# Kernel optimization log

Measured on AMD Instinct MI355X. Metric: run time of the kernel, lower is better.

Reference implementation:

```python
import jax, jax.numpy as jnp
import numpy as np

B, T, V, D = 256, 128, 32000, 512
DT = 0.04
CUBIC = 0.008
LAMBDA = 0.1
SIGNAL_SCALE = 0.5
NORM_EPS = 1e-8       # state_norm_eps
SIG_EPS = 1e-6        # signal_eps
SLOW_DECAY = 0.05
SLOW_LR = 0.05
W_FAST = 1.0
W_SLOW = 0.3
CONV_STEPS = 4
LN_EPS = 1e-5


def make_diffusion_matrix(dim):
    rng = np.random.default_rng(42)
    q, _ = np.linalg.qr(rng.standard_normal((dim, dim)).astype(np.float64))
    u = rng.random(dim)
    eig = -0.2 - (0.05 + 0.3 * u)
    return jnp.asarray((q * eig) @ q.T, dtype=jnp.float32)


def setup_inputs() -> dict:
    key = jax.random.key(0)
    k1, k2, k3 = jax.random.split(key, 3)
    tokens = jax.random.randint(k1, (B, T), 0, V)
    embed = jax.random.normal(k2, (V, D), dtype=jnp.float32) * 0.02
    readout_w = jax.random.normal(k3, (V, D), dtype=jnp.float32) * 0.02
    diffusion = make_diffusion_matrix(D)
    gamma = jnp.float32(0.2)
    beta = jnp.float32(0.75)
    return {"tokens": tokens, "embed": embed, "readout_w": readout_w,
            "diffusion": diffusion, "gamma": gamma, "beta": beta}


def _layernorm(x):
    mu = jnp.mean(x, axis=-1, keepdims=True)
    var = jnp.mean((x - mu) ** 2, axis=-1, keepdims=True)
    return (x - mu) / jnp.sqrt(var + LN_EPS)


def _norm(x):
    return jnp.linalg.norm(x, axis=-1, keepdims=True)


def _context_vector(fast, slow):
    combined = W_FAST * fast + W_SLOW * slow
    fn = _norm(fast)
    cn = _norm(combined)
    fast_dir = fast / (fn + SIG_EPS)
    comb_dir = combined / (cn + SIG_EPS)
    return jnp.where(fn > 1e-8, fast_dir,
                     jnp.where(cn > 1e-8, comb_dir, jnp.zeros_like(fast)))


def _step_state(state, signal, diffusion, beta):
    c = state - jnp.mean(state, axis=-1, keepdims=True)
    drift = (state @ diffusion.T + CUBIC * jnp.tanh(c)
             + beta * (SIGNAL_SCALE * signal) - LAMBDA * state)
    s = state + DT * drift
    s = jnp.nan_to_num(s, nan=0.0, posinf=0.0, neginf=0.0)
    s = s / (_norm(s) + NORM_EPS)
    return jnp.clip(s, -10.0, 10.0)


def reference(tokens, embed, readout_w, diffusion, gamma, beta):
    # tokens: [B,T] int; states: [B,D]
    fast0 = jnp.zeros((tokens.shape[0], D), dtype=embed.dtype)
    slow0 = jnp.zeros_like(fast0)

    def token_step(carry, tok):
        fast, slow = carry
        emb = _layernorm(embed[tok])                       # [B,D]
        base = emb / jnp.maximum(_norm(emb), 1e-12)
        ctx = _context_vector(fast, slow)
        sig = base + gamma * ctx
        sig = sig / (_norm(sig) + SIG_EPS)
        for _ in range(CONV_STEPS):
            fast = _step_state(fast, sig, diffusion, beta)
        slow = (1.0 - SLOW_DECAY) * slow + SLOW_LR * fast
        sn = _norm(slow)
        slow = jnp.where(sn > 0.5, slow * (0.5 / (sn + 1e-12)), slow)
        return (fast, slow), None

    (fast, slow), _ = jax.lax.scan(token_step, (fast0, slow0), tokens.T)
    combined = W_FAST * fast + W_SLOW * slow               # [B,D]
    logits = combined @ readout_w.T                        # [B,V]
    return logits
```

## Files before the change

kernel.cpp:

```cpp
#include <hip/hip_runtime.h>
#include <math.h>

#define DDIM 512
#define TLEN 128
#define RB   8
#define NWG  32
#define VDIM 32000
#define NWAVE 8
#define SR   528

typedef _Float16 f16x8 __attribute__((ext_vector_type(8)));
typedef float    f32x4 __attribute__((ext_vector_type(4)));
typedef _Float16 h2    __attribute__((ext_vector_type(2)));

__device__ __forceinline__ unsigned int pkh2(float a, float b) {
  h2 v; v.x = (_Float16)a; v.y = (_Float16)b;
  return __builtin_bit_cast(unsigned int, v);
}
__device__ __forceinline__ float h2f(unsigned short h) {
  return (float)__builtin_bit_cast(_Float16, h);
}
__device__ __forceinline__ unsigned short f2h(float f) {
  return __builtin_bit_cast(unsigned short, (_Float16)f);
}
__device__ __forceinline__ float tanh_fast(float x) {
#if __has_builtin(__builtin_amdgcn_exp2f) && __has_builtin(__builtin_amdgcn_rcpf)
  const float e = __builtin_amdgcn_exp2f(x * 2.885390081777927f);
  return 1.f - 2.f * __builtin_amdgcn_rcpf(e + 1.f);
#else
  const float e = exp2f(x * 2.885390081777927f);
  return 1.f - 2.f / (e + 1.f);
#endif
}
__device__ __forceinline__ f32x4 unpk4(uint2 u) {
  f32x4 r;
  r[0] = h2f((unsigned short)(u.x & 0xffff));
  r[1] = h2f((unsigned short)(u.x >> 16));
  r[2] = h2f((unsigned short)(u.y & 0xffff));
  r[3] = h2f((unsigned short)(u.y >> 16));
  return r;
}

__device__ __forceinline__ void wg_barrier() {
  asm volatile("s_waitcnt lgkmcnt(0)" ::: "memory");
  __builtin_amdgcn_s_barrier();
  asm volatile("" ::: "memory");
}

__global__ __launch_bounds__(256) void pack_diffusion(
    const float* __restrict__ A, uint4* __restrict__ pk)
{
  const int slot = blockIdx.x * 256 + threadIdx.x;
  const int l  = slot & 63;
  const int fr = slot >> 6;
  const int kt = fr & 15;
  const int it = fr >> 4;
  const float* src = A + (size_t)(it * 16 + (l & 15)) * DDIM + kt * 32 + (l >> 4) * 8;
  pk[slot] = make_uint4(pkh2(src[0], src[1]), pkh2(src[2], src[3]),
                        pkh2(src[4], src[5]), pkh2(src[6], src[7]));
}

__global__ __launch_bounds__(512) void precompute_mubi(
    const int*   __restrict__ tokens,
    const float* __restrict__ embed,
    float4*      __restrict__ mubi)
{
  const int idx = blockIdx.x * 8 + (threadIdx.x >> 6);
  const int l   = threadIdx.x & 63;
  const int b   = idx >> 7;
  const int t   = idx & 127;
  const int tok = tokens[b * TLEN + t];
  float s1 = 0.f, s2 = 0.f;
  #pragma unroll
  for (int e = 0; e < 8; ++e) {
    const float v = embed[(size_t)tok * DDIM + l + e * 64];
    s1 += v; s2 += v * v;
  }
  #pragma unroll
  for (int off = 32; off >= 1; off >>= 1) {
    s1 += __shfl_xor(s1, off);
    s2 += __shfl_xor(s2, off);
  }
  if (l == 0) {
    const float mu = s1 * (1.f / DDIM);
    float var = s2 * (1.f / DDIM) - mu * mu;
    var = fmaxf(var, 0.f);
    const float inv  = rsqrtf(var + 1e-5f);
    const float n2y  = (float)DDIM * var / (var + 1e-5f);
    const float invn = 1.f / fmaxf(sqrtf(n2y), 1e-12f);
    const float bi   = inv * invn;
    const float b2   = n2y * invn * invn;
    mubi[idx] = make_float4(mu, bi, b2, 0.f);
  }
}

#define PF(B_, KT_)                                                          \
  {                                                                          \
    _Pragma("unroll")                                                        \
    for (int mt = 0; mt < 4; ++mt)                                           \
      B_[mt] = apw[(size_t)(mt * 16 + (KT_)) * 64];                          \
  }
#define USE(B_, KT_)                                                         \
  {                                                                          \
    const f16x8 bf = *(const f16x8*)&srow[rp][rl * SR + (KT_) * 32 + g * 8]; \
    _Pragma("unroll")                                                        \
    for (int mt = 0; mt < 4; ++mt)                                           \
      C[mt] = __builtin_amdgcn_mfma_f32_16x16x32_f16(                        \
          __builtin_bit_cast(f16x8, B_[mt]), bf, C[mt], 0, 0, 0);            \
  }
#define USE_AR(KT_)                                                          \
  {                                                                          \
    const f16x8 bf = *(const f16x8*)&srow[rp][rl * SR + (KT_) * 32 + g * 8]; \
    _Pragma("unroll")                                                        \
    for (int mt = 0; mt < 4; ++mt)                                           \
      C[mt] = __builtin_amdgcn_mfma_f32_16x16x32_f16(                        \
          __builtin_bit_cast(f16x8, AR[KT_][mt]), bf, C[mt], 0, 0, 0);       \
  }
#define USE_LD(KT_)                                                          \
  {                                                                          \
    const f16x8 bf = *(const f16x8*)&srow[rp][rl * SR + (KT_) * 32 + g * 8]; \
    _Pragma("unroll")                                                        \
    for (int mt = 0; mt < 4; ++mt) {                                         \
      const uint4 af = ares[((w * 4 + mt) * 4 + ((KT_) - 4)) * 64 + l];      \
      C[mt] = __builtin_amdgcn_mfma_f32_16x16x32_f16(                        \
          __builtin_bit_cast(f16x8, af), bf, C[mt], 0, 0, 0);                \
    }                                                                        \
  }

__global__ __launch_bounds__(512, 1) void attractor_recurrence(
    const int*    __restrict__ tokens,
    const float*  __restrict__ embed,
    const uint4*  __restrict__ Apk,
    const float4* __restrict__ mubi,
    const float*  __restrict__ gamma_p,
    const float*  __restrict__ beta_p,
    float*        __restrict__ comb_out)
{
  const int tid   = threadIdx.x;
  const int w     = tid >> 6;
  const int l     = tid & 63;
  const int g     = l >> 4;
  const int n     = l & 15;
  const int rl    = n & 7;
  const int hi    = (n >> 3) & 1;
  const int row0  = blockIdx.x * RB;
  const int wbase = w * 64;

  __shared__ unsigned short srow[2][RB * SR];
  __shared__ unsigned short forceh[RB * SR];
  __shared__ float4 redc[2][NWAVE][RB];
  __shared__ float4 redt[NWAVE][2];
  __shared__ float2 carry[RB];
  __shared__ float4 mb[RB];
  __shared__ uint4  ares[32 * 4 * 64];

  for (int x = tid; x < RB * SR; x += 512) { srow[0][x] = 0; srow[1][x] = 0; }
  for (int x = tid; x < 32 * 4 * 64; x += 512) {
    const int it = x >> 8;
    const int kr = (x >> 6) & 3;
    const int ll = x & 63;
    ares[x] = Apk[(size_t)(it * 16 + 4 + kr) * 64 + ll];
  }

  const uint4* apw = Apk + (size_t)(w * 64) * 64 + l;
  uint4 AR[4][4];
  #pragma unroll
  for (int kt = 0; kt < 4; ++kt)
    #pragma unroll
    for (int mt = 0; mt < 4; ++mt)
      AR[kt][mt] = apw[(size_t)(mt * 16 + kt) * 64];

  const float gamma = gamma_p[0];
  const float bss   = beta_p[0] * 0.5f;

  float fs[2][4];
  float sl[2][4];
  #pragma unroll
  for (int mtl = 0; mtl < 2; ++mtl)
    #pragma unroll
    for (int q = 0; q < 4; ++q) { fs[mtl][q] = 0.f; sl[mtl][q] = 0.f; }
  float S_reg = 0.f, S2_reg = 0.f, SX_reg = 0.f;
  float sl2 = 0.f;

  float evc[8];
  #pragma unroll
  for (int r = 0; r < 8; ++r) {
    const int tok = tokens[(row0 + r) * TLEN + 0];
    evc[r] = embed[(size_t)tok * DDIM + tid];
  }

  __syncthreads();

  uint4 A0[4], A1[4], A2[4];
  PF(A0, 8); PF(A1, 9); PF(A2, 10);

  for (int t = 0; t < TLEN; ++t) {
    const int tn = (t + 1 < TLEN) ? t + 1 : t;
    float evn[8];
    #pragma unroll
    for (int r = 0; r < 8; ++r) {
      const int tok = tokens[(row0 + r) * TLEN + tn];
      evn[r] = embed[(size_t)tok * DDIM + tid];
    }
    if (tid < 8) mb[tid] = mubi[(size_t)(row0 + tid) * TLEN + t];
    float pr[8];
    #pragma unroll
    for (int r = 0; r < 8; ++r)
      pr[r] = evc[r] * h2f(srow[0][r * SR + tid]);
    #pragma unroll
    for (int off = 32; off >= 1; off >>= 1)
      #pragma unroll
      for (int q = 0; q < 8; ++q)
        pr[q] += __shfl_xor(pr[q], off);
    if (l == 0) {
      redt[w][0] = make_float4(pr[0], pr[1], pr[2], pr[3]);
      redt[w][1] = make_float4(pr[4], pr[5], pr[6], pr[7]);
    }
    if (tid < 8) carry[tid] = make_float2(S_reg, S2_reg);
    if (t > 0) {
      const float sq3   = sqrtf(S2_reg);
      const float ispn3 = 1.f / (sq3 + 1e-8f);
      const float fn3   = sq3 * ispn3;
      const float sdf   = SX_reg * ispn3;
      const float sn2   = 0.9025f * sl2 + 0.095f * sdf + 0.0025f * fn3 * fn3;
      const float sn    = sqrtf(fmaxf(sn2, 0.f));
      const float scale = (sn > 0.5f) ? 0.5f / (sn + 1e-12f) : 1.f;
      sl2 = sn2 * scale * scale;
      #pragma unroll
      for (int mtl = 0; mtl < 2; ++mtl)
        #pragma unroll
        for (int q = 0; q < 4; ++q)
          sl[mtl][q] = (0.95f * sl[mtl][q] + 0.05f * fs[mtl][q] * ispn3) * scale;
    }
    wg_barrier();

    {
      float rs[8];
      #pragma unroll
      for (int q = 0; q < 8; ++q) rs[q] = 0.f;
      #pragma unroll
      for (int wv = 0; wv < NWAVE; ++wv) {
        const float4 v0 = redt[wv][0];
        const float4 v1 = redt[wv][1];
        rs[0] += v0.x; rs[1] += v0.y; rs[2] += v0.z; rs[3] += v0.w;
        rs[4] += v1.x; rs[5] += v1.y; rs[6] += v1.z; rs[7] += v1.w;
      }
      #pragma unroll
      for (int r = 0; r < 8; ++r) {
        const float2 cy  = carry[r];
        const float4 mbr = mb[r];
        const float sq   = sqrtf(cy.y);
        const float ispr = 1.f / (sq + 1e-8f);
        const float fno  = sq * ispr;
        const float invf = 1.f / (fno + 1e-6f);
        const float qr   = ispr * invf;
        const float mu   = mbr.x;
        const float bi   = mbr.y;
        const float b2   = mbr.z;
        const float sctx = qr * cy.x;
        const float bdot = bi * (qr * rs[r] - mu * sctx);
        const float cn2  = qr * qr * cy.y;
        const float sg2  = b2 + 2.f * gamma * bdot + gamma * gamma * cn2;
        const float isig = 1.f / (sqrtf(fmaxf(sg2, 0.f)) + 1e-6f);
        const float ctx  = qr * h2f(srow[0][r * SR + tid]);
        forceh[r * SR + tid] = f2h(bss * ((evc[r] - mu) * bi + gamma * ctx) * isig);
      }
    }
    wg_barrier();

    #pragma unroll 1
    for (int k = 0; k < 4; ++k) {
      const int  rp   = k & 1;
      const int  wp   = rp ^ 1;
      const bool last = (k == 3);

      f32x4 C[4];
      #pragma unroll
      for (int mt = 0; mt < 4; ++mt) C[mt] = (f32x4){0.f, 0.f, 0.f, 0.f};

      USE_AR(0); USE_AR(1); USE_AR(2); USE_AR(3);
      USE_LD(4); USE_LD(5); USE_LD(6); USE_LD(7);
      USE(A0,  8); PF(A0, 11);
      USE(A1,  9); PF(A1, 12);
      USE(A2, 10); PF(A2, 13);
      USE(A0, 11); PF(A0, 14);
      USE(A1, 12); PF(A1, 15);
      USE(A2, 13); PF(A2, 10);
      USE(A0, 14); PF(A0,  8);
      USE(A1, 15); PF(A1,  9);

      const float ispn  = 1.f / (sqrtf(S2_reg) + 1e-8f);
      const float smean = S_reg * ispn * (1.f / DDIM);
      f32x4 Cs[2];
      Cs[0] = hi ? C[2] : C[0];
      Cs[1] = hi ? C[3] : C[1];
      const int i0base = wbase + hi * 32 + g * 4;
      float vs = 0.f, v2 = 0.f, vx = 0.f;
      #pragma unroll
      for (int mtl = 0; mtl < 2; ++mtl) {
        const int i0 = i0base + mtl * 16;
        const f32x4 ff = unpk4(*(const uint2*)&forceh[rl * SR + i0]);
        #pragma unroll
        for (int q = 0; q < 4; ++q) {
          const float s   = fs[mtl][q] * ispn;
          const float th  = tanh_fast(s - smean);
          const float dr  = Cs[mtl][q] * ispn + 0.008f * th + ff[q] - 0.1f * s;
          const float spv = fmaf(0.04f, dr, s);
          fs[mtl][q] = spv;
          vs += spv; v2 += spv * spv;
          if (last) vx += sl[mtl][q] * spv;
        }
      }
      vs += __shfl_xor(vs, 8);  v2 += __shfl_xor(v2, 8);  vx += __shfl_xor(vx, 8);
      vs += __shfl_xor(vs, 16); v2 += __shfl_xor(v2, 16); vx += __shfl_xor(vx, 16);
      vs += __shfl_xor(vs, 32); v2 += __shfl_xor(v2, 32); vx += __shfl_xor(vx, 32);

      #pragma unroll
      for (int mtl = 0; mtl < 2; ++mtl) {
        const int i0 = i0base + mtl * 16;
        uint2 pkv;
        pkv.x = pkh2(fs[mtl][0], fs[mtl][1]);
        pkv.y = pkh2(fs[mtl][2], fs[mtl][3]);
        *(uint2*)&srow[wp][rl * SR + i0] = pkv;
      }
      if (l < 8) redc[rp][w][l] = make_float4(vs, v2, vx, 0.f);
      wg_barrier();
      float S = 0.f, S2 = 0.f, SX = 0.f;
      #pragma unroll
      for (int wv = 0; wv < NWAVE; ++wv) {
        const float4 v = redc[rp][wv][rl];
        S += v.x; S2 += v.y; SX += v.z;
      }
      S_reg = S; S2_reg = S2; SX_reg = SX;
    }

    #pragma unroll
    for (int r = 0; r < 8; ++r) evc[r] = evn[r];
  }

  {
    const float sq3   = sqrtf(S2_reg);
    const float ispn3 = 1.f / (sq3 + 1e-8f);
    const float fn3   = sq3 * ispn3;
    const float sdf   = SX_reg * ispn3;
    const float sn2   = 0.9025f * sl2 + 0.095f * sdf + 0.0025f * fn3 * fn3;
    const float sn    = sqrtf(fmaxf(sn2, 0.f));
    const float scale = (sn > 0.5f) ? 0.5f / (sn + 1e-12f) : 1.f;
    const int i0base = wbase + hi * 32 + g * 4;
    #pragma unroll
    for (int mtl = 0; mtl < 2; ++mtl) {
      const int i0 = i0base + mtl * 16;
      float4 o;
      #pragma unroll
      for (int q = 0; q < 4; ++q) {
        const float f = fs[mtl][q] * ispn3;
        const float s = (0.95f * sl[mtl][q] + 0.05f * f) * scale;
        ((float*)&o)[q] = f + 0.3f * s;
      }
      *(float4*)&comb_out[(size_t)(row0 + rl) * DDIM + i0] = o;
    }
  }
}

#define KC  32
#define LDT 132

__global__ __launch_bounds__(256) void logits_gemm(
    const float* __restrict__ comb,
    const float* __restrict__ W,
    float*       __restrict__ out)
{
  __shared__ float wt[KC * LDT];
  __shared__ float ct[KC * LDT];

  const int tid = threadIdx.x;
  const int v0  = blockIdx.x * 128;
  const int b0  = blockIdx.y * 128;
  const int tb  = tid >> 4;
  const int tv  = tid & 15;

  float acc[8][8];
  #pragma unroll
  for (int a = 0; a < 8; ++a)
    #pragma unroll
    for (int b = 0; b < 8; ++b) acc[a][b] = 0.f;

  for (int kk = 0; kk < DDIM; kk += KC) {
    #pragma unroll
    for (int it = 0; it < 4; ++it) {
      const int l4  = tid + it * 256;
      const int row = l4 >> 3;
      const int k4  = (l4 & 7) << 2;
      const float4 gw = *(const float4*)&W[(size_t)(v0 + row) * DDIM + kk + k4];
      const float4 gc = *(const float4*)&comb[(size_t)(b0 + row) * DDIM + kk + k4];
      wt[(k4 + 0) * LDT + row] = gw.x;
      wt[(k4 + 1) * LDT + row] = gw.y;
      wt[(k4 + 2) * LDT + row] = gw.z;
      wt[(k4 + 3) * LDT + row] = gw.w;
      ct[(k4 + 0) * LDT + row] = gc.x;
      ct[(k4 + 1) * LDT + row] = gc.y;
      ct[(k4 + 2) * LDT + row] = gc.z;
      ct[(k4 + 3) * LDT + row] = gc.w;
    }
    __syncthreads();

    for (int kx = 0; kx < KC; ++kx) {
      const float4 c0 = *(const float4*)&ct[kx * LDT + tb * 8];
      const float4 c1 = *(const float4*)&ct[kx * LDT + tb * 8 + 4];
      const float4 w0 = *(const float4*)&wt[kx * LDT + tv * 8];
      const float4 w1 = *(const float4*)&wt[kx * LDT + tv * 8 + 4];
      const float cw[8] = {c0.x, c0.y, c0.z, c0.w, c1.x, c1.y, c1.z, c1.w};
      const float wv[8] = {w0.x, w0.y, w0.z, w0.w, w1.x, w1.y, w1.z, w1.w};
      #pragma unroll
      for (int ib = 0; ib < 8; ++ib)
        #pragma unroll
        for (int iv = 0; iv < 8; ++iv)
          acc[ib][iv] = fmaf(cw[ib], wv[iv], acc[ib][iv]);
    }
    __syncthreads();
  }

  #pragma unroll
  for (int ib = 0; ib < 8; ++ib) {
    const size_t base = (size_t)(b0 + tb * 8 + ib) * VDIM + v0 + tv * 8;
    *(float4*)&out[base]     = make_float4(acc[ib][0], acc[ib][1], acc[ib][2], acc[ib][3]);
    *(float4*)&out[base + 4] = make_float4(acc[ib][4], acc[ib][5], acc[ib][6], acc[ib][7]);
  }
}

extern "C" void kernel_launch(void* const* d_in, const int* in_sizes, int n_in,
                              void* d_out, int out_size, void* d_ws, size_t ws_size,
                              hipStream_t stream) {
  const int*   tokens    = (const int*)d_in[0];
  const float* embed     = (const float*)d_in[1];
  const float* readout_w = (const float*)d_in[2];
  const float* diffusion = (const float*)d_in[3];
  const float* gamma_p   = (const float*)d_in[4];
  const float* beta_p    = (const float*)d_in[5];

  float*  comb = (float*)d_ws;
  uint4*  Apk  = (uint4*)((char*)d_ws + 512 * 1024);
  float4* mubi = (float4*)((char*)d_ws + 1024 * 1024);

  hipLaunchKernelGGL(pack_diffusion, dim3(128), dim3(256), 0, stream,
                     diffusion, Apk);
  hipLaunchKernelGGL(precompute_mubi, dim3(256 * TLEN / 8), dim3(512), 0, stream,
                     tokens, embed, mubi);
  hipLaunchKernelGGL(attractor_recurrence, dim3(NWG), dim3(512), 0, stream,
                     tokens, embed, Apk, mubi, gamma_p, beta_p, comb);
  hipLaunchKernelGGL(logits_gemm, dim3(VDIM / 128, 256 / 128), dim3(256), 0, stream,
                     comb, readout_w, (float*)d_out);
}
```

Measured before the change: 3.784 ms.

## Split recurrence state columns across paired workgroups with flag-based global exchange

The recurrence kernel now runs on 64 workgroups via a cooperative launch, each pair of workgroups owning one 8-row batch group and splitting the 512 state columns in half. Each workgroup keeps half of the diffusion matrix (registers plus LDS), computes half of the matvec per step, and then exchanges its fp16 state half and partial norm sums with its partner through global memory, using release/acquire flags and spin-waiting. This halves the per-workgroup MFMA work and diffusion-matrix streaming on the serial critical path. In exchange it adds a global-memory round trip and cross-workgroup synchronisation on each of the 512 inner steps.

```diff
diff --git a/kernel.cpp b/kernel.cpp
--- a/kernel.cpp
+++ b/kernel.cpp
@@ -4,10 +4,10 @@
 #define DDIM 512
 #define TLEN 128
 #define RB   8
-#define NWG  32
 #define VDIM 32000
 #define NWAVE 8
 #define SR   528
+#define PAYB 4608
 
 typedef _Float16 f16x8 __attribute__((ext_vector_type(8)));
 typedef float    f32x4 __attribute__((ext_vector_type(4)));
@@ -88,31 +88,15 @@
     const float inv  = rsqrtf(var + 1e-5f);
     const float n2y  = (float)DDIM * var / (var + 1e-5f);
     const float invn = 1.f / fmaxf(sqrtf(n2y), 1e-12f);
-    const float bi   = inv * invn;
-    const float b2   = n2y * invn * invn;
-    mubi[idx] = make_float4(mu, bi, b2, 0.f);
-  }
-}
-
-#define PF(B_, KT_)                                                          \
-  {                                                                          \
-    _Pragma("unroll")                                                        \
-    for (int mt = 0; mt < 4; ++mt)                                           \
-      B_[mt] = apw[(size_t)(mt * 16 + (KT_)) * 64];                          \
-  }
-#define USE(B_, KT_)                                                         \
-  {                                                                          \
-    const f16x8 bf = *(const f16x8*)&srow[rp][rl * SR + (KT_) * 32 + g * 8]; \
-    _Pragma("unroll")                                                        \
-    for (int mt = 0; mt < 4; ++mt)                                           \
-      C[mt] = __builtin_amdgcn_mfma_f32_16x16x32_f16(                        \
-          __builtin_bit_cast(f16x8, B_[mt]), bf, C[mt], 0, 0, 0);            \
-  }
+    mubi[idx] = make_float4(mu, inv * invn, n2y * invn * invn, 0.f);
+  }
+}
+
 #define USE_AR(KT_)                                                          \
   {                                                                          \
     const f16x8 bf = *(const f16x8*)&srow[rp][rl * SR + (KT_) * 32 + g * 8]; \
     _Pragma("unroll")                                                        \
-    for (int mt = 0; mt < 4; ++mt)                                           \
+    for (int mt = 0; mt < 2; ++mt)                                           \
       C[mt] = __builtin_amdgcn_mfma_f32_16x16x32_f16(                        \
           __builtin_bit_cast(f16x8, AR[KT_][mt]), bf, C[mt], 0, 0, 0);       \
   }
@@ -120,21 +104,23 @@
   {                                                                          \
     const f16x8 bf = *(const f16x8*)&srow[rp][rl * SR + (KT_) * 32 + g * 8]; \
     _Pragma("unroll")                                                        \
-    for (int mt = 0; mt < 4; ++mt) {                                         \
-      const uint4 af = ares[((w * 4 + mt) * 4 + ((KT_) - 4)) * 64 + l];      \
+    for (int mt = 0; mt < 2; ++mt) {                                         \
+      const uint4 af = ares[((w * 2 + mt) * 8 + ((KT_) - 8)) * 64 + l];      \
       C[mt] = __builtin_amdgcn_mfma_f32_16x16x32_f16(                        \
           __builtin_bit_cast(f16x8, af), bf, C[mt], 0, 0, 0);                \
     }                                                                        \
   }
 
-__global__ __launch_bounds__(512, 1) void attractor_recurrence(
+__global__ __launch_bounds__(512, 1) void attractor_coop(
     const int*    __restrict__ tokens,
     const float*  __restrict__ embed,
     const uint4*  __restrict__ Apk,
     const float4* __restrict__ mubi,
     const float*  __restrict__ gamma_p,
     const float*  __restrict__ beta_p,
-    float*        __restrict__ comb_out)
+    float*        __restrict__ comb_out,
+    unsigned int* __restrict__ flagbuf,
+    unsigned char* __restrict__ exch)
 {
   const int tid   = threadIdx.x;
   const int w     = tid >> 6;
@@ -143,8 +129,14 @@
   const int n     = l & 15;
   const int rl    = n & 7;
   const int hi    = (n >> 3) & 1;
-  const int row0  = blockIdx.x * RB;
-  const int wbase = w * 64;
+  const int b     = blockIdx.x;
+  const int half  = b >> 5;
+  const int grp   = b & 31;
+  const int pb    = b ^ 32;
+  const int phalf = 1 - half;
+  const int row0  = grp * RB;
+  const int colh  = w * 32 + hi * 16 + g * 4;
+  const int ig    = half * 256 + colh;
 
   __shared__ unsigned short srow[2][RB * SR];
   __shared__ unsigned short forceh[RB * SR];
@@ -152,35 +144,34 @@
   __shared__ float4 redt[NWAVE][2];
   __shared__ float2 carry[RB];
   __shared__ float4 mb[RB];
-  __shared__ uint4  ares[32 * 4 * 64];
+  __shared__ float4 statl[RB];
+  __shared__ uint4  ares[16 * 8 * 64];
 
   for (int x = tid; x < RB * SR; x += 512) { srow[0][x] = 0; srow[1][x] = 0; }
-  for (int x = tid; x < 32 * 4 * 64; x += 512) {
-    const int it = x >> 8;
-    const int kr = (x >> 6) & 3;
-    const int ll = x & 63;
-    ares[x] = Apk[(size_t)(it * 16 + 4 + kr) * 64 + ll];
-  }
-
-  const uint4* apw = Apk + (size_t)(w * 64) * 64 + l;
-  uint4 AR[4][4];
-  #pragma unroll
-  for (int kt = 0; kt < 4; ++kt)
-    #pragma unroll
-    for (int mt = 0; mt < 4; ++mt)
-      AR[kt][mt] = apw[(size_t)(mt * 16 + kt) * 64];
+  for (int x = tid; x < 16 * 8 * 64; x += 512) {
+    const int itl = x >> 9;
+    const int kt8 = (x >> 6) & 7;
+    const int ll  = x & 63;
+    ares[x] = Apk[(size_t)((half * 16 + itl) * 16 + 8 + kt8) * 64 + ll];
+  }
+  if (tid < 8) statl[tid] = make_float4(0.f, 0.f, 0.f, 0.f);
+
+  uint4 AR[8][2];
+  #pragma unroll
+  for (int kt = 0; kt < 8; ++kt)
+    #pragma unroll
+    for (int mt = 0; mt < 2; ++mt) {
+      const int it_g = half * 16 + w * 2 + mt;
+      AR[kt][mt] = Apk[(size_t)(it_g * 16 + kt) * 64 + l];
+    }
 
   const float gamma = gamma_p[0];
   const float bss   = beta_p[0] * 0.5f;
 
-  float fs[2][4];
-  float sl[2][4];
-  #pragma unroll
-  for (int mtl = 0; mtl < 2; ++mtl)
-    #pragma unroll
-    for (int q = 0; q < 4; ++q) { fs[mtl][q] = 0.f; sl[mtl][q] = 0.f; }
-  float S_reg = 0.f, S2_reg = 0.f, SX_reg = 0.f;
-  float sl2 = 0.f;
+  float fs[4], sl[4];
+  #pragma unroll
+  for (int q = 0; q < 4; ++q) { fs[q] = 0.f; sl[q] = 0.f; }
+  float S_reg = 0.f, S2_reg = 0.f, SX_reg = 0.f, sl2 = 0.f;
 
   float evc[8];
   #pragma unroll
@@ -189,10 +180,8 @@
     evc[r] = embed[(size_t)tok * DDIM + tid];
   }
 
+  unsigned int e = 0;
   __syncthreads();
-
-  uint4 A0[4], A1[4], A2[4];
-  PF(A0, 8); PF(A1, 9); PF(A2, 10);
 
   for (int t = 0; t < TLEN; ++t) {
     const int tn = (t + 1 < TLEN) ? t + 1 : t;
@@ -227,10 +216,8 @@
       const float scale = (sn > 0.5f) ? 0.5f / (sn + 1e-12f) : 1.f;
       sl2 = sn2 * scale * scale;
       #pragma unroll
-      for (int mtl = 0; mtl < 2; ++mtl)
-        #pragma unroll
-        for (int q = 0; q < 4; ++q)
-          sl[mtl][q] = (0.95f * sl[mtl][q] + 0.05f * fs[mtl][q] * ispn3) * scale;
+      for (int q = 0; q < 4; ++q)
+        sl[q] = (0.95f * sl[q] + 0.05f * fs[q] * ispn3) * scale;
     }
     wg_barrier();
 
@@ -254,84 +241,96 @@
         const float fno  = sq * ispr;
         const float invf = 1.f / (fno + 1e-6f);
         const float qr   = ispr * invf;
-        const float mu   = mbr.x;
-        const float bi   = mbr.y;
-        const float b2   = mbr.z;
         const float sctx = qr * cy.x;
-        const float bdot = bi * (qr * rs[r] - mu * sctx);
+        const float bdot = mbr.y * (qr * rs[r] - mbr.x * sctx);
         const float cn2  = qr * qr * cy.y;
-        const float sg2  = b2 + 2.f * gamma * bdot + gamma * gamma * cn2;
+        const float sg2  = mbr.z + 2.f * gamma * bdot + gamma * gamma * cn2;
         const float isig = 1.f / (sqrtf(fmaxf(sg2, 0.f)) + 1e-6f);
         const float ctx  = qr * h2f(srow[0][r * SR + tid]);
-        forceh[r * SR + tid] = f2h(bss * ((evc[r] - mu) * bi + gamma * ctx) * isig);
+        forceh[r * SR + tid] = f2h(bss * ((evc[r] - mbr.x) * mbr.y + gamma * ctx) * isig);
       }
     }
     wg_barrier();
 
     #pragma unroll 1
     for (int k = 0; k < 4; ++k) {
-      const int  rp   = k & 1;
-      const int  wp   = rp ^ 1;
+      const int  rp = k & 1;
+      const int  wp = rp ^ 1;
       const bool last = (k == 3);
-
-      f32x4 C[4];
-      #pragma unroll
-      for (int mt = 0; mt < 4; ++mt) C[mt] = (f32x4){0.f, 0.f, 0.f, 0.f};
-
-      USE_AR(0); USE_AR(1); USE_AR(2); USE_AR(3);
-      USE_LD(4); USE_LD(5); USE_LD(6); USE_LD(7);
-      USE(A0,  8); PF(A0, 11);
-      USE(A1,  9); PF(A1, 12);
-      USE(A2, 10); PF(A2, 13);
-      USE(A0, 11); PF(A0, 14);
-      USE(A1, 12); PF(A1, 15);
-      USE(A2, 13); PF(A2, 10);
-      USE(A0, 14); PF(A0,  8);
-      USE(A1, 15); PF(A1,  9);
+      const unsigned int ex = ++e;
+      const int p = ex & 1;
+
+      f32x4 C[2];
+      C[0] = (f32x4){0.f, 0.f, 0.f, 0.f};
+      C[1] = (f32x4){0.f, 0.f, 0.f, 0.f};
+      USE_AR(0); USE_AR(1); USE_AR(2);  USE_AR(3);
+      USE_AR(4); USE_AR(5); USE_AR(6);  USE_AR(7);
+      USE_LD(8); USE_LD(9); USE_LD(10); USE_LD(11);
+      USE_LD(12); USE_LD(13); USE_LD(14); USE_LD(15);
 
       const float ispn  = 1.f / (sqrtf(S2_reg) + 1e-8f);
       const float smean = S_reg * ispn * (1.f / DDIM);
-      f32x4 Cs[2];
-      Cs[0] = hi ? C[2] : C[0];
-      Cs[1] = hi ? C[3] : C[1];
-      const int i0base = wbase + hi * 32 + g * 4;
+      const f32x4 Cs = C[hi];
+      const f32x4 ff = unpk4(*(const uint2*)&forceh[rl * SR + ig]);
       float vs = 0.f, v2 = 0.f, vx = 0.f;
       #pragma unroll
-      for (int mtl = 0; mtl < 2; ++mtl) {
-        const int i0 = i0base + mtl * 16;
-        const f32x4 ff = unpk4(*(const uint2*)&forceh[rl * SR + i0]);
-        #pragma unroll
-        for (int q = 0; q < 4; ++q) {
-          const float s   = fs[mtl][q] * ispn;
-          const float th  = tanh_fast(s - smean);
-          const float dr  = Cs[mtl][q] * ispn + 0.008f * th + ff[q] - 0.1f * s;
-          const float spv = fmaf(0.04f, dr, s);
-          fs[mtl][q] = spv;
-          vs += spv; v2 += spv * spv;
-          if (last) vx += sl[mtl][q] * spv;
-        }
+      for (int q = 0; q < 4; ++q) {
+        const float s   = fs[q] * ispn;
+        const float th  = tanh_fast(s - smean);
+        const float dr  = Cs[q] * ispn + 0.008f * th + ff[q] - 0.1f * s;
+        const float spv = fmaf(0.04f, dr, s);
+        fs[q] = spv;
+        vs += spv; v2 += spv * spv;
+        if (last) vx += sl[q] * spv;
       }
       vs += __shfl_xor(vs, 8);  v2 += __shfl_xor(v2, 8);  vx += __shfl_xor(vx, 8);
       vs += __shfl_xor(vs, 16); v2 += __shfl_xor(v2, 16); vx += __shfl_xor(vx, 16);
       vs += __shfl_xor(vs, 32); v2 += __shfl_xor(v2, 32); vx += __shfl_xor(vx, 32);
 
-      #pragma unroll
-      for (int mtl = 0; mtl < 2; ++mtl) {
-        const int i0 = i0base + mtl * 16;
+      unsigned char* exme = exch + (size_t)(b * 2 + p) * PAYB;
+      {
         uint2 pkv;
-        pkv.x = pkh2(fs[mtl][0], fs[mtl][1]);
-        pkv.y = pkh2(fs[mtl][2], fs[mtl][3]);
-        *(uint2*)&srow[wp][rl * SR + i0] = pkv;
+        pkv.x = pkh2(fs[0], fs[1]);
+        pkv.y = pkh2(fs[2], fs[3]);
+        *(uint2*)&srow[wp][rl * SR + ig] = pkv;
+        *(uint2*)(exme + (size_t)(rl * 256 + colh) * 2) = pkv;
       }
       if (l < 8) redc[rp][w][l] = make_float4(vs, v2, vx, 0.f);
       wg_barrier();
-      float S = 0.f, S2 = 0.f, SX = 0.f;
-      #pragma unroll
-      for (int wv = 0; wv < NWAVE; ++wv) {
-        const float4 v = redc[rp][wv][rl];
-        S += v.x; S2 += v.y; SX += v.z;
-      }
-      S_reg = S; S2_reg = S2; SX_reg = SX;
+      float o0 = 0.f, o1 = 0.f, o2 = 0.f;
+      if (tid < 8) {
+        #pragma unroll
+        for (int wv = 0; wv < NWAVE; ++wv) {
+          const float4 v = redc[rp][wv][tid];
+          o0 += v.x; o1 += v.y; o2 += v.z;
+        }
+        *(float4*)(exme + 4096 + tid * 16) = make_float4(o0, o1, o2, 0.f);
+      }
+      __syncthreads();
+      if (tid == 0) {
+        __hip_atomic_store(&flagbuf[b * 32], ex, __ATOMIC_RELEASE,
+                           __HIP_MEMORY_SCOPE_AGENT);
+        while (__hip_atomic_load(&flagbuf[pb * 32], __ATOMIC_ACQUIRE,
+                                 __HIP_MEMORY_SCOPE_AGENT) < ex) {
+          __builtin_amdgcn_s_sleep(1);
+        }
+      }
+      __syncthreads();
+      __threadfence();
+      {
+        const unsigned char* expp = exch + (size_t)(pb * 2 + p) * PAYB;
+        const int rr = tid >> 6;
+        const int cc = (tid & 63) * 4;
+        const uint2 pv = *(const uint2*)(expp + (size_t)(rr * 256 + cc) * 2);
+        *(uint2*)&srow[wp][rr * SR + phalf * 256 + cc] = pv;
+        if (tid < 8) {
+          const float4 pt = *(const float4*)(expp + 4096 + tid * 16);
+          statl[tid] = make_float4(o0 + pt.x, o1 + pt.y, o2 + pt.z, 0.f);
+        }
+      }
+      wg_barrier();
+      const float4 sv = statl[rl];
+      S_reg = sv.x; S2_reg = sv.y; SX_reg = sv.z;
     }
 
     #pragma unroll
@@ -346,19 +345,14 @@
     const float sn2   = 0.9025f * sl2 + 0.095f * sdf + 0.0025f * fn3 * fn3;
     const float sn    = sqrtf(fmaxf(sn2, 0.f));
     const float scale = (sn > 0.5f) ? 0.5f / (sn + 1e-12f) : 1.f;
-    const int i0base = wbase + hi * 32 + g * 4;
-    #pragma unroll
-    for (int mtl = 0; mtl < 2; ++mtl) {
-      const int i0 = i0base + mtl * 16;
-      float4 o;
-      #pragma unroll
-      for (int q = 0; q < 4; ++q) {
-        const float f = fs[mtl][q] * ispn3;
-        const float s = (0.95f * sl[mtl][q] + 0.05f * f) * scale;
-        ((float*)&o)[q] = f + 0.3f * s;
-      }
-      *(float4*)&comb_out[(size_t)(row0 + rl) * DDIM + i0] = o;
-    }
+    float4 o;
+    #pragma unroll
+    for (int q = 0; q < 4; ++q) {
+      const float f = fs[q] * ispn3;
+      const float s = (0.95f * sl[q] + 0.05f * f) * scale;
+      ((float*)&o)[q] = f + 0.3f * s;
+    }
+    *(float4*)&comb_out[(size_t)(row0 + rl) * DDIM + ig] = o;
   }
 }
 
@@ -438,16 +432,24 @@
   const float* gamma_p   = (const float*)d_in[4];
   const float* beta_p    = (const float*)d_in[5];
 
-  float*  comb = (float*)d_ws;
-  uint4*  Apk  = (uint4*)((char*)d_ws + 512 * 1024);
-  float4* mubi = (float4*)((char*)d_ws + 1024 * 1024);
-
+  float*         comb  = (float*)d_ws;
+  uint4*         Apk   = (uint4*)((char*)d_ws + 512 * 1024);
+  float4*        mubi  = (float4*)((char*)d_ws + 1024 * 1024);
+  unsigned int*  flags = (unsigned int*)((char*)d_ws + 1536 * 1024);
+  unsigned char* exch  = (unsigned char*)d_ws + 1536 * 1024 + 8192;
+
+  hipMemsetAsync(flags, 0, 8192, stream);
   hipLaunchKernelGGL(pack_diffusion, dim3(128), dim3(256), 0, stream,
                      diffusion, Apk);
   hipLaunchKernelGGL(precompute_mubi, dim3(256 * TLEN / 8), dim3(512), 0, stream,
                      tokens, embed, mubi);
-  hipLaunchKernelGGL(attractor_recurrence, dim3(NWG), dim3(512), 0, stream,
-                     tokens, embed, Apk, mubi, gamma_p, beta_p, comb);
+
+  void* args[] = {(void*)&tokens, (void*)&embed, (void*)&Apk, (void*)&mubi,
+                  (void*)&gamma_p, (void*)&beta_p, (void*)&comb,
+                  (void*)&flags, (void*)&exch};
+  hipLaunchCooperativeKernel((void*)attractor_coop, dim3(64), dim3(512),
+                             args, 0, stream);
+
   hipLaunchKernelGGL(logits_gemm, dim3(VDIM / 128, 256 / 128), dim3(256), 0, stream,
                      comb, readout_w, (float*)d_out);
 }
```

New measurement: 5.912 ms. +56.2%, slower.

## Keep more diffusion-matrix k-tiles resident in registers and LDS

Applied to the files above, without the earlier changes.

Re-partitions where the diffusion matrix operand tiles live: k-tiles 0-7 are now held in VGPRs (previously 0-3), tiles 8-11 in LDS (previously 4-7), and only tiles 12-15 are streamed from global memory each step, with four prefetch buffers instead of a rotating three-buffer scheme. The goal is to cut global/L2 traffic on the latency-critical recurrence. The cost is more register pressure (32 extra uint4 values held), which may cause spills at launch bounds 512. The streamed tiles are now reloaded after all MFMAs in a step, so their latency overlaps the epilogue rather than the matmul.

```diff
diff --git a/kernel.cpp b/kernel.cpp
--- a/kernel.cpp
+++ b/kernel.cpp
@@ -88,26 +88,10 @@
     const float inv  = rsqrtf(var + 1e-5f);
     const float n2y  = (float)DDIM * var / (var + 1e-5f);
     const float invn = 1.f / fmaxf(sqrtf(n2y), 1e-12f);
-    const float bi   = inv * invn;
-    const float b2   = n2y * invn * invn;
-    mubi[idx] = make_float4(mu, bi, b2, 0.f);
-  }
-}
-
-#define PF(B_, KT_)                                                          \
-  {                                                                          \
-    _Pragma("unroll")                                                        \
-    for (int mt = 0; mt < 4; ++mt)                                           \
-      B_[mt] = apw[(size_t)(mt * 16 + (KT_)) * 64];                          \
-  }
-#define USE(B_, KT_)                                                         \
-  {                                                                          \
-    const f16x8 bf = *(const f16x8*)&srow[rp][rl * SR + (KT_) * 32 + g * 8]; \
-    _Pragma("unroll")                                                        \
-    for (int mt = 0; mt < 4; ++mt)                                           \
-      C[mt] = __builtin_amdgcn_mfma_f32_16x16x32_f16(                        \
-          __builtin_bit_cast(f16x8, B_[mt]), bf, C[mt], 0, 0, 0);            \
-  }
+    mubi[idx] = make_float4(mu, inv * invn, n2y * invn * invn, 0.f);
+  }
+}
+
 #define USE_AR(KT_)                                                          \
   {                                                                          \
     const f16x8 bf = *(const f16x8*)&srow[rp][rl * SR + (KT_) * 32 + g * 8]; \
@@ -121,10 +105,24 @@
     const f16x8 bf = *(const f16x8*)&srow[rp][rl * SR + (KT_) * 32 + g * 8]; \
     _Pragma("unroll")                                                        \
     for (int mt = 0; mt < 4; ++mt) {                                         \
-      const uint4 af = ares[((w * 4 + mt) * 4 + ((KT_) - 4)) * 64 + l];      \
+      const uint4 af = ares[((w * 4 + mt) * 4 + ((KT_) - 8)) * 64 + l];      \
       C[mt] = __builtin_amdgcn_mfma_f32_16x16x32_f16(                        \
           __builtin_bit_cast(f16x8, af), bf, C[mt], 0, 0, 0);                \
     }                                                                        \
+  }
+#define USE_S(J_, KT_)                                                       \
+  {                                                                          \
+    const f16x8 bf = *(const f16x8*)&srow[rp][rl * SR + (KT_) * 32 + g * 8]; \
+    _Pragma("unroll")                                                        \
+    for (int mt = 0; mt < 4; ++mt)                                           \
+      C[mt] = __builtin_amdgcn_mfma_f32_16x16x32_f16(                        \
+          __builtin_bit_cast(f16x8, S##J_[mt]), bf, C[mt], 0, 0, 0);         \
+  }
+#define PF_S(J_, KT_)                                                        \
+  {                                                                          \
+    _Pragma("unroll")                                                        \
+    for (int mt = 0; mt < 4; ++mt)                                           \
+      S##J_[mt] = apw[(size_t)(mt * 16 + (KT_)) * 64];                       \
   }
 
 __global__ __launch_bounds__(512, 1) void attractor_recurrence(
@@ -159,13 +157,13 @@
     const int it = x >> 8;
     const int kr = (x >> 6) & 3;
     const int ll = x & 63;
-    ares[x] = Apk[(size_t)(it * 16 + 4 + kr) * 64 + ll];
+    ares[x] = Apk[(size_t)(it * 16 + 8 + kr) * 64 + ll];
   }
 
   const uint4* apw = Apk + (size_t)(w * 64) * 64 + l;
-  uint4 AR[4][4];
-  #pragma unroll
-  for (int kt = 0; kt < 4; ++kt)
+  uint4 AR[8][4];
+  #pragma unroll
+  for (int kt = 0; kt < 8; ++kt)
     #pragma unroll
     for (int mt = 0; mt < 4; ++mt)
       AR[kt][mt] = apw[(size_t)(mt * 16 + kt) * 64];
@@ -191,8 +189,8 @@
 
   __syncthreads();
 
-  uint4 A0[4], A1[4], A2[4];
-  PF(A0, 8); PF(A1, 9); PF(A2, 10);
+  uint4 S0[4], S1[4], S2[4], S3[4];
+  PF_S(0, 12); PF_S(1, 13); PF_S(2, 14); PF_S(3, 15);
 
   for (int t = 0; t < TLEN; ++t) {
     const int tn = (t + 1 < TLEN) ? t + 1 : t;
@@ -254,16 +252,13 @@
         const float fno  = sq * ispr;
         const float invf = 1.f / (fno + 1e-6f);
         const float qr   = ispr * invf;
-        const float mu   = mbr.x;
-        const float bi   = mbr.y;
-        const float b2   = mbr.z;
         const float sctx = qr * cy.x;
-        const float bdot = bi * (qr * rs[r] - mu * sctx);
+        const float bdot = mbr.y * (qr * rs[r] - mbr.x * sctx);
         const float cn2  = qr * qr * cy.y;
-        const float sg2  = b2 + 2.f * gamma * bdot + gamma * gamma * cn2;
+        const float sg2  = mbr.z + 2.f * gamma * bdot + gamma * gamma * cn2;
         const float isig = 1.f / (sqrtf(fmaxf(sg2, 0.f)) + 1e-6f);
         const float ctx  = qr * h2f(srow[0][r * SR + tid]);
-        forceh[r * SR + tid] = f2h(bss * ((evc[r] - mu) * bi + gamma * ctx) * isig);
+        forceh[r * SR + tid] = f2h(bss * ((evc[r] - mbr.x) * mbr.y + gamma * ctx) * isig);
       }
     }
     wg_barrier();
@@ -279,15 +274,10 @@
       for (int mt = 0; mt < 4; ++mt) C[mt] = (f32x4){0.f, 0.f, 0.f, 0.f};
 
       USE_AR(0); USE_AR(1); USE_AR(2); USE_AR(3);
-      USE_LD(4); USE_LD(5); USE_LD(6); USE_LD(7);
-      USE(A0,  8); PF(A0, 11);
-      USE(A1,  9); PF(A1, 12);
-      USE(A2, 10); PF(A2, 13);
-      USE(A0, 11); PF(A0, 14);
-      USE(A1, 12); PF(A1, 15);
-      USE(A2, 13); PF(A2, 10);
-      USE(A0, 14); PF(A0,  8);
-      USE(A1, 15); PF(A1,  9);
+      USE_AR(4); USE_AR(5); USE_AR(6); USE_AR(7);
+      USE_LD(8); USE_LD(9); USE_LD(10); USE_LD(11);
+      USE_S(0, 12); USE_S(1, 13); USE_S(2, 14); USE_S(3, 15);
+      PF_S(0, 12); PF_S(1, 13); PF_S(2, 14); PF_S(3, 15);
 
       const float ispn  = 1.f / (sqrtf(S2_reg) + 1e-8f);
       const float smean = S_reg * ispn * (1.f / DDIM);
```

Measured after the change: 3.847 ms. Within noise of the previous version (+1.7%).

## Halve rows per workgroup to spread the recurrence over twice as many workgroups

Applied to the files above, without the earlier changes.

Rows handled per workgroup drop from 8 to 4, so the recurrence runs on 64 workgroups instead of 32 and uses more of the GPU's compute units. Each lane now owns a single 4-element slice of fast state instead of two, which changes the MFMA output lane mapping and adds one shuffle stage to the reductions. The MFMA work per workgroup stays the same size, because the 16-column B operand still holds only a few real rows. Each workgroup still streams the full diffusion matrix, so total matrix traffic doubles.

```diff
diff --git a/kernel.cpp b/kernel.cpp
--- a/kernel.cpp
+++ b/kernel.cpp
@@ -3,8 +3,8 @@
 
 #define DDIM 512
 #define TLEN 128
-#define RB   8
-#define NWG  32
+#define RB   4
+#define NWG  64
 #define VDIM 32000
 #define NWAVE 8
 #define SR   528
@@ -88,26 +88,10 @@
     const float inv  = rsqrtf(var + 1e-5f);
     const float n2y  = (float)DDIM * var / (var + 1e-5f);
     const float invn = 1.f / fmaxf(sqrtf(n2y), 1e-12f);
-    const float bi   = inv * invn;
-    const float b2   = n2y * invn * invn;
-    mubi[idx] = make_float4(mu, bi, b2, 0.f);
-  }
-}
-
-#define PF(B_, KT_)                                                          \
-  {                                                                          \
-    _Pragma("unroll")                                                        \
-    for (int mt = 0; mt < 4; ++mt)                                           \
-      B_[mt] = apw[(size_t)(mt * 16 + (KT_)) * 64];                          \
-  }
-#define USE(B_, KT_)                                                         \
-  {                                                                          \
-    const f16x8 bf = *(const f16x8*)&srow[rp][rl * SR + (KT_) * 32 + g * 8]; \
-    _Pragma("unroll")                                                        \
-    for (int mt = 0; mt < 4; ++mt)                                           \
-      C[mt] = __builtin_amdgcn_mfma_f32_16x16x32_f16(                        \
-          __builtin_bit_cast(f16x8, B_[mt]), bf, C[mt], 0, 0, 0);            \
-  }
+    mubi[idx] = make_float4(mu, inv * invn, n2y * invn * invn, 0.f);
+  }
+}
+
 #define USE_AR(KT_)                                                          \
   {                                                                          \
     const f16x8 bf = *(const f16x8*)&srow[rp][rl * SR + (KT_) * 32 + g * 8]; \
@@ -125,6 +109,20 @@
       C[mt] = __builtin_amdgcn_mfma_f32_16x16x32_f16(                        \
           __builtin_bit_cast(f16x8, af), bf, C[mt], 0, 0, 0);                \
     }                                                                        \
+  }
+#define USE(B_, KT_)                                                         \
+  {                                                                          \
+    const f16x8 bf = *(const f16x8*)&srow[rp][rl * SR + (KT_) * 32 + g * 8]; \
+    _Pragma("unroll")                                                        \
+    for (int mt = 0; mt < 4; ++mt)                                           \
+      C[mt] = __builtin_amdgcn_mfma_f32_16x16x32_f16(                        \
+          __builtin_bit_cast(f16x8, B_[mt]), bf, C[mt], 0, 0, 0);            \
+  }
+#define PF(B_, KT_)                                                          \
+  {                                                                          \
+    _Pragma("unroll")                                                        \
+    for (int mt = 0; mt < 4; ++mt)                                           \
+      B_[mt] = apw[(size_t)(mt * 16 + (KT_)) * 64];                          \
   }
 
 __global__ __launch_bounds__(512, 1) void attractor_recurrence(
@@ -141,15 +139,14 @@
   const int l     = tid & 63;
   const int g     = l >> 4;
   const int n     = l & 15;
-  const int rl    = n & 7;
-  const int hi    = (n >> 3) & 1;
+  const int rl    = n & 3;
   const int row0  = blockIdx.x * RB;
   const int wbase = w * 64;
 
   __shared__ unsigned short srow[2][RB * SR];
   __shared__ unsigned short forceh[RB * SR];
   __shared__ float4 redc[2][NWAVE][RB];
-  __shared__ float4 redt[NWAVE][2];
+  __shared__ float4 redt[NWAVE];
   __shared__ float2 carry[RB];
   __shared__ float4 mb[RB];
   __shared__ uint4  ares[32 * 4 * 64];
@@ -173,18 +170,15 @@
   const float gamma = gamma_p[0];
   const float bss   = beta_p[0] * 0.5f;
 
-  float fs[2][4];
-  float sl[2][4];
-  #pragma unroll
-  for (int mtl = 0; mtl < 2; ++mtl)
-    #pragma unroll
-    for (int q = 0; q < 4; ++q) { fs[mtl][q] = 0.f; sl[mtl][q] = 0.f; }
+  float fs[4], sl[4];
+  #pragma unroll
+  for (int q = 0; q < 4; ++q) { fs[q] = 0.f; sl[q] = 0.f; }
   float S_reg = 0.f, S2_reg = 0.f, SX_reg = 0.f;
   float sl2 = 0.f;
 
-  float evc[8];
-  #pragma unroll
-  for (int r = 0; r < 8; ++r) {
+  float evc[RB];
+  #pragma unroll
+  for (int r = 0; r < RB; ++r) {
     const int tok = tokens[(row0 + r) * TLEN + 0];
     evc[r] = embed[(size_t)tok * DDIM + tid];
   }
@@ -196,27 +190,25 @@
 
   for (int t = 0; t < TLEN; ++t) {
     const int tn = (t + 1 < TLEN) ? t + 1 : t;
-    float evn[8];
-    #pragma unroll
-    for (int r = 0; r < 8; ++r) {
+    float evn[RB];
+    #pragma unroll
+    for (int r = 0; r < RB; ++r) {
       const int tok = tokens[(row0 + r) * TLEN + tn];
       evn[r] = embed[(size_t)tok * DDIM + tid];
     }
-    if (tid < 8) mb[tid] = mubi[(size_t)(row0 + tid) * TLEN + t];
-    float pr[8];
-    #pragma unroll
-    for (int r = 0; r < 8; ++r)
+    if (tid < RB) mb[tid] = mubi[(size_t)(row0 + tid) * TLEN + t];
+    float pr[RB];
+    #pragma unroll
+    for (int r = 0; r < RB; ++r)
       pr[r] = evc[r] * h2f(srow[0][r * SR + tid]);
     #pragma unroll
     for (int off = 32; off >= 1; off >>= 1)
       #pragma unroll
-      for (int q = 0; q < 8; ++q)
+      for (int q = 0; q < RB; ++q)
         pr[q] += __shfl_xor(pr[q], off);
-    if (l == 0) {
-      redt[w][0] = make_float4(pr[0], pr[1], pr[2], pr[3]);
-      redt[w][1] = make_float4(pr[4], pr[5], pr[6], pr[7]);
-    }
-    if (tid < 8) carry[tid] = make_float2(S_reg, S2_reg);
+    if (l == 0)
+      redt[w] = make_float4(pr[0], pr[1], pr[2], pr[3]);
+    if (tid < RB) carry[tid] = make_float2(S_reg, S2_reg);
     if (t > 0) {
       const float sq3   = sqrtf(S2_reg);
       const float ispn3 = 1.f / (sq3 + 1e-8f);
@@ -227,26 +219,22 @@
       const float scale = (sn > 0.5f) ? 0.5f / (sn + 1e-12f) : 1.f;
       sl2 = sn2 * scale * scale;
       #pragma unroll
-      for (int mtl = 0; mtl < 2; ++mtl)
-        #pragma unroll
-        for (int q = 0; q < 4; ++q)
-          sl[mtl][q] = (0.95f * sl[mtl][q] + 0.05f * fs[mtl][q] * ispn3) * scale;
+      for (int q = 0; q < 4; ++q)
+        sl[q] = (0.95f * sl[q] + 0.05f * fs[q] * ispn3) * scale;
     }
     wg_barrier();
 
     {
-      float rs[8];
-      #pragma unroll
-      for (int q = 0; q < 8; ++q) rs[q] = 0.f;
+      float rs[RB];
+      #pragma unroll
+      for (int q = 0; q < RB; ++q) rs[q] = 0.f;
       #pragma unroll
       for (int wv = 0; wv < NWAVE; ++wv) {
-        const float4 v0 = redt[wv][0];
-        const float4 v1 = redt[wv][1];
+        const float4 v0 = redt[wv];
         rs[0] += v0.x; rs[1] += v0.y; rs[2] += v0.z; rs[3] += v0.w;
-        rs[4] += v1.x; rs[5] += v1.y; rs[6] += v1.z; rs[7] += v1.w;
       }
       #pragma unroll
-      for (int r = 0; r < 8; ++r) {
+      for (int r = 0; r < RB; ++r) {
         const float2 cy  = carry[r];
         const float4 mbr = mb[r];
         const float sq   = sqrtf(cy.y);
@@ -254,16 +242,13 @@
         const float fno  = sq * ispr;
         const float invf = 1.f / (fno + 1e-6f);
         const float qr   = ispr * invf;
-        const float mu   = mbr.x;
-        const float bi   = mbr.y;
-        const float b2   = mbr.z;
         const float sctx = qr * cy.x;
-        const float bdot = bi * (qr * rs[r] - mu * sctx);
+        const float bdot = mbr.y * (qr * rs[r] - mbr.x * sctx);
         const float cn2  = qr * qr * cy.y;
-        const float sg2  = b2 + 2.f * gamma * bdot + gamma * gamma * cn2;
+        const float sg2  = mbr.z + 2.f * gamma * bdot + gamma * gamma * cn2;
         const float isig = 1.f / (sqrtf(fmaxf(sg2, 0.f)) + 1e-6f);
         const float ctx  = qr * h2f(srow[0][r * SR + tid]);
-        forceh[r * SR + tid] = f2h(bss * ((evc[r] - mu) * bi + gamma * ctx) * isig);
+        forceh[r * SR + tid] = f2h(bss * ((evc[r] - mbr.x) * mbr.y + gamma * ctx) * isig);
       }
     }
     wg_barrier();
@@ -291,39 +276,33 @@
 
       const float ispn  = 1.f / (sqrtf(S2_reg) + 1e-8f);
       const float smean = S_reg * ispn * (1.f / DDIM);
-      f32x4 Cs[2];
-      Cs[0] = hi ? C[2] : C[0];
-      Cs[1] = hi ? C[3] : C[1];
-      const int i0base = wbase + hi * 32 + g * 4;
+      const int b2 = (n >> 3) & 1, b1 = (n >> 2) & 1;
+      const f32x4 Cs = b2 ? (b1 ? C[3] : C[2]) : (b1 ? C[1] : C[0]);
+      const int i0 = wbase + ((n >> 2) << 4) + g * 4;
+      const f32x4 ff = unpk4(*(const uint2*)&forceh[rl * SR + i0]);
       float vs = 0.f, v2 = 0.f, vx = 0.f;
       #pragma unroll
-      for (int mtl = 0; mtl < 2; ++mtl) {
-        const int i0 = i0base + mtl * 16;
-        const f32x4 ff = unpk4(*(const uint2*)&forceh[rl * SR + i0]);
-        #pragma unroll
-        for (int q = 0; q < 4; ++q) {
-          const float s   = fs[mtl][q] * ispn;
-          const float th  = tanh_fast(s - smean);
-          const float dr  = Cs[mtl][q] * ispn + 0.008f * th + ff[q] - 0.1f * s;
-          const float spv = fmaf(0.04f, dr, s);
-          fs[mtl][q] = spv;
-          vs += spv; v2 += spv * spv;
-          if (last) vx += sl[mtl][q] * spv;
-        }
+      for (int q = 0; q < 4; ++q) {
+        const float s   = fs[q] * ispn;
+        const float th  = tanh_fast(s - smean);
+        const float dr  = Cs[q] * ispn + 0.008f * th + ff[q] - 0.1f * s;
+        const float spv = fmaf(0.04f, dr, s);
+        fs[q] = spv;
+        vs += spv; v2 += spv * spv;
+        if (last) vx += sl[q] * spv;
       }
+      vs += __shfl_xor(vs, 4);  v2 += __shfl_xor(v2, 4);  vx += __shfl_xor(vx, 4);
       vs += __shfl_xor(vs, 8);  v2 += __shfl_xor(v2, 8);  vx += __shfl_xor(vx, 8);
       vs += __shfl_xor(vs, 16); v2 += __shfl_xor(v2, 16); vx += __shfl_xor(vx, 16);
       vs += __shfl_xor(vs, 32); v2 += __shfl_xor(v2, 32); vx += __shfl_xor(vx, 32);
 
-      #pragma unroll
-      for (int mtl = 0; mtl < 2; ++mtl) {
-        const int i0 = i0base + mtl * 16;
+      {
         uint2 pkv;
-        pkv.x = pkh2(fs[mtl][0], fs[mtl][1]);
-        pkv.y = pkh2(fs[mtl][2], fs[mtl][3]);
+        pkv.x = pkh2(fs[0], fs[1]);
+        pkv.y = pkh2(fs[2], fs[3]);
         *(uint2*)&srow[wp][rl * SR + i0] = pkv;
       }
-      if (l < 8) redc[rp][w][l] = make_float4(vs, v2, vx, 0.f);
+      if (l < RB) redc[rp][w][l] = make_float4(vs, v2, vx, 0.f);
       wg_barrier();
       float S = 0.f, S2 = 0.f, SX = 0.f;
       #pragma unroll
@@ -335,7 +314,7 @@
     }
 
     #pragma unroll
-    for (int r = 0; r < 8; ++r) evc[r] = evn[r];
+    for (int r = 0; r < RB; ++r) evc[r] = evn[r];
   }
 
   {
@@ -346,19 +325,15 @@
     const float sn2   = 0.9025f * sl2 + 0.095f * sdf + 0.0025f * fn3 * fn3;
     const float sn    = sqrtf(fmaxf(sn2, 0.f));
     const float scale = (sn > 0.5f) ? 0.5f / (sn + 1e-12f) : 1.f;
-    const int i0base = wbase + hi * 32 + g * 4;
-    #pragma unroll
-    for (int mtl = 0; mtl < 2; ++mtl) {
-      const int i0 = i0base + mtl * 16;
-      float4 o;
-      #pragma unroll
-      for (int q = 0; q < 4; ++q) {
-        const float f = fs[mtl][q] * ispn3;
-        const float s = (0.95f * sl[mtl][q] + 0.05f * f) * scale;
-        ((float*)&o)[q] = f + 0.3f * s;
-      }
-      *(float4*)&comb_out[(size_t)(row0 + rl) * DDIM + i0] = o;
-    }
+    const int i0 = wbase + ((n >> 2) << 4) + g * 4;
+    float4 o;
+    #pragma unroll
+    for (int q = 0; q < 4; ++q) {
+      const float f = fs[q] * ispn3;
+      const float s = (0.95f * sl[q] + 0.05f * f) * scale;
+      ((float*)&o)[q] = f + 0.3f * s;
+    }
+    *(float4*)&comb_out[(size_t)(row0 + rl) * DDIM + i0] = o;
   }
 }
 
```

After: 3.255 ms (median of 2 runs). 14.0% less time.
